# Kernel tuning notes

Hardware: AMD Instinct MI355X
Metric: run time of the kernel (lower is better)

## Reference

```python
import jax, jax.numpy as jnp
import numpy as np


def setup_inputs() -> dict:
    key = jax.random.key(0)
    x = jax.random.normal(key, (16, 64, 256, 256), dtype=jnp.float32)
    return {"x": x}


def reference(x) -> jnp.ndarray:
    B, C, H, W = x.shape
    hw = H * W
    q = x.reshape(B, C, hw)          # proj_query: [B, C, HW]
    k = x.reshape(B, hw, C)          # proj_key: view (reshape), NOT transpose — faithful to source
    attn = jax.nn.softmax(jnp.einsum('bcn,bnd->bcd', q, k), axis=-1)  # [B, C, C]
    out = jnp.einsum('bcd,bdn->bcn', attn, q).reshape(B, C, H, W)
    return out + x
```

## Files before the change

kernel.cpp:

```cpp
#include <hip/hip_runtime.h>

#define B_   16
#define C_   64
#define HW_  65536
#define CHW_ (C_ * HW_)
#define XSTRIDE 260

typedef short bf16x8 __attribute__((ext_vector_type(8)));
typedef float f32x4v __attribute__((ext_vector_type(4)));

__device__ __forceinline__ unsigned short bfrne(float f) {
    unsigned int u = __float_as_uint(f);
    u += 0x7FFFu + ((u >> 16) & 1u);
    return (unsigned short)(u >> 16);
}
__device__ __forceinline__ float bfdec(unsigned short h) {
    return __uint_as_float((unsigned int)h << 16);
}

__global__ __launch_bounds__(256, 2) void k1_gram(const float* __restrict__ x,
                                                  float* __restrict__ partial,
                                                  int nch, int nb) {
    const int ch  = blockIdx.x;
    const int b   = blockIdx.y;
    const int t   = threadIdx.x;
    const int w   = t >> 6;
    const int l   = t & 63;
    const int g   = l >> 4;
    const int col = l & 15;

    __shared__ float Bs[4][2][2048];

    const float* xb = x + (size_t)b * CHW_;
    const int nq  = nb >> 2;
    const int nw0 = ch * nb + w * nq;
    const int nit = nq >> 5;

#define K1_STAGE(dst, ns)                                                  \
    {                                                                      \
        const float* bsrc = xb + (size_t)(ns) * C_;                        \
        _Pragma("unroll")                                                  \
        for (int i = 0; i < 8; i++) {                                      \
            const int sw = (i >> 1) << 2;                                  \
            const float* gp = bsrc + 256 * i + 64 * (l >> 4)               \
                              + 4 * ((l & 15) ^ sw);                       \
            __builtin_amdgcn_global_load_lds(                              \
                (const __attribute__((address_space(1))) void*)gp,         \
                (__attribute__((address_space(3))) void*)((dst) + 256 * i),\
                16, 0, 0);                                                 \
        }                                                                  \
    }

#define K1_LOADA(AV, ns)                                                   \
    _Pragma("unroll")                                                      \
    for (int ct = 0; ct < 4; ct++) {                                       \
        const float* ap = xb + (size_t)(16 * ct + col) * HW_ + (ns) + 8 * g; \
        *(float4*)&AV[ct][0] = *(const float4*)ap;                         \
        *(float4*)&AV[ct][4] = *(const float4*)(ap + 4);                   \
    }

#define K1_CONVA(AV)                                                       \
    _Pragma("unroll")                                                      \
    for (int ct = 0; ct < 4; ct++)                                         \
        _Pragma("unroll")                                                  \
        for (int j = 0; j < 8; j++) {                                      \
            const unsigned short h = bfrne(AV[ct][j]);                     \
            ahi[ct][j] = (short)h;                                         \
            alo[ct][j] = (short)bfrne(AV[ct][j] - bfdec(h));               \
        }

#define K1_BPHASE(cur)                                                     \
    _Pragma("unroll")                                                      \
    for (int dt = 0; dt < 4; dt++) {                                       \
        const int eo = 16 * (dt ^ g) + col;                                \
        float bv[8];                                                       \
        _Pragma("unroll")                                                  \
        for (int j = 0; j < 8; j++) bv[j] = (cur)[(8 * g + j) * 64 + eo];  \
        bf16x8 bhi, blo;                                                   \
        _Pragma("unroll")                                                  \
        for (int j = 0; j < 8; j++) {                                      \
            const unsigned short h = bfrne(bv[j]);                         \
            bhi[j] = (short)h;                                             \
            blo[j] = (short)bfrne(bv[j] - bfdec(h));                       \
        }                                                                  \
        _Pragma("unroll")                                                  \
        for (int ct = 0; ct < 4; ct++) {                                   \
            acc[ct][dt] = __builtin_amdgcn_mfma_f32_16x16x32_bf16(         \
                ahi[ct], bhi, acc[ct][dt], 0, 0, 0);                       \
            acc[ct][dt] = __builtin_amdgcn_mfma_f32_16x16x32_bf16(         \
                ahi[ct], blo, acc[ct][dt], 0, 0, 0);                       \
            acc[ct][dt] = __builtin_amdgcn_mfma_f32_16x16x32_bf16(         \
                alo[ct], bhi, acc[ct][dt], 0, 0, 0);                       \
        }                                                                  \
    }

    f32x4v acc[4][4];
    #pragma unroll
    for (int ct = 0; ct < 4; ct++)
        #pragma unroll
        for (int dt = 0; dt < 4; dt++) acc[ct][dt] = (f32x4v)(0.f);

    float avA[4][8], avB[4][8];
    bf16x8 ahi[4], alo[4];

    K1_STAGE(Bs[w][0], nw0);
    K1_LOADA(avA, nw0);

    for (int it2 = 0; it2 < nit; it2 += 2) {
        {
            const int ns = nw0 + (it2 << 5);
            K1_LOADA(avB, ns + 32);
            K1_STAGE(Bs[w][1], ns + 32);
            K1_CONVA(avA);
            asm volatile("s_waitcnt vmcnt(16)" ::: "memory");
            K1_BPHASE(Bs[w][0]);
        }
        {
            const int ns = nw0 + ((it2 + 1) << 5);
            if (it2 + 2 < nit) {
                K1_LOADA(avA, ns + 32);
                K1_STAGE(Bs[w][0], ns + 32);
            }
            K1_CONVA(avB);
            if (it2 + 2 < nit) asm volatile("s_waitcnt vmcnt(16)" ::: "memory");
            else               asm volatile("s_waitcnt vmcnt(0)"  ::: "memory");
            K1_BPHASE(Bs[w][1]);
        }
    }
#undef K1_STAGE
#undef K1_LOADA
#undef K1_CONVA
#undef K1_BPHASE

    float* sred = (float*)Bs;
    for (int wr = 0; wr < 4; wr++) {
        if (w == wr) {
            #pragma unroll
            for (int ct = 0; ct < 4; ct++)
                #pragma unroll
                for (int dt = 0; dt < 4; dt++)
                    #pragma unroll
                    for (int r = 0; r < 4; r++) {
                        const int idx = (16 * ct + 4 * g + r) * 64 + 16 * dt + col;
                        if (wr == 0) sred[idx] = acc[ct][dt][r];
                        else         sred[idx] += acc[ct][dt][r];
                    }
        }
        __syncthreads();
    }

    float* pb = partial + (size_t)(b * nch + ch) * 4096;
    for (int i = 4 * t; i < 4096; i += 1024)
        *(float4*)&pb[i] = *(const float4*)&sred[i];
}

__global__ __launch_bounds__(256) void k2_softmax(const float* __restrict__ partial,
                                                  unsigned short* __restrict__ mbf,
                                                  int nch) {
    const int c = blockIdx.x;
    const int b = blockIdx.y;
    const int t = threadIdx.x;
    const int w = t >> 6;
    const int d = t & 63;

    float s = 0.f;
    for (int ch = w; ch < nch; ch += 4)
        s += partial[(size_t)(b * nch + ch) * 4096 + c * 64 + d];

    __shared__ float red[256];
    red[t] = s;
    __syncthreads();
    if (w == 0) {
        s = red[d] + red[64 + d] + red[128 + d] + red[192 + d];
        float m = s;
        #pragma unroll
        for (int off = 32; off > 0; off >>= 1) m = fmaxf(m, __shfl_xor(m, off));
        const float e = expf(s - m);
        float sum = e;
        #pragma unroll
        for (int off = 32; off > 0; off >>= 1) sum += __shfl_xor(sum, off);
        mbf[(size_t)b * 4096 + c * 64 + d] = bfrne(e / sum + (c == d ? 1.f : 0.f));
    }
}

__global__ __launch_bounds__(256, 2) void k3_out(const float* __restrict__ x,
                                                 const unsigned short* __restrict__ mbf,
                                                 float* __restrict__ out) {
    const int nbk = blockIdx.x;
    const int b   = blockIdx.y;
    const int t   = threadIdx.x;
    const int w   = t >> 6;
    const int l   = t & 63;
    const int g   = l >> 4;
    const int col = l & 15;

    __shared__ float Xs[64 * XSTRIDE];

    const int nblk = nbk * 256;
    const float* xb = x + (size_t)b * CHW_;

    #pragma unroll
    for (int i = 0; i < 16; i++) {
        const int d = 16 * w + i;
        const int p = ((d >> 3) & 1) << 2;
        const float* gp = xb + (size_t)d * HW_ + nblk + 4 * (l ^ p);
        __builtin_amdgcn_global_load_lds(
            (const __attribute__((address_space(1))) void*)gp,
            (__attribute__((address_space(3))) void*)(&Xs[d * XSTRIDE]),
            16, 0, 0);
    }

    bf16x8 afr[4][2];
    const unsigned short* mb = mbf + (size_t)b * 4096;
    #pragma unroll
    for (int ct = 0; ct < 4; ct++)
        #pragma unroll
        for (int ks = 0; ks < 2; ks++)
            afr[ct][ks] = *(const bf16x8*)(mb + (16 * ct + col) * 64 + 32 * ks + 8 * g);

    __syncthreads();

    f32x4v acc[4][4];
    #pragma unroll
    for (int ct = 0; ct < 4; ct++)
        #pragma unroll
        for (int nt = 0; nt < 4; nt++)
            acc[ct][nt] = (f32x4v)(0.f);

    const int psw = (g & 1) << 2;

    #pragma unroll
    for (int nt = 0; nt < 4; nt++) {
        const int n  = 64 * w + 16 * nt + col;
        const int cn = n >> 2;
        const int eo = ((cn ^ psw) << 2) + (col & 3);

        bf16x8 bfr[2];
        #pragma unroll
        for (int ks = 0; ks < 2; ks++)
            #pragma unroll
            for (int j = 0; j < 8; j++) {
                const int r = 32 * ks + 8 * g + j;
                bfr[ks][j] = (short)bfrne(Xs[r * XSTRIDE + eo]);
            }

        #pragma unroll
        for (int ct = 0; ct < 4; ct++)
            #pragma unroll
            for (int ks = 0; ks < 2; ks++)
                acc[ct][nt] = __builtin_amdgcn_mfma_f32_16x16x32_bf16(
                    afr[ct][ks], bfr[ks], acc[ct][nt], 0, 0, 0);
    }

    __syncthreads();
    #pragma unroll
    for (int ct = 0; ct < 4; ct++)
        #pragma unroll
        for (int nt = 0; nt < 4; nt++)
            #pragma unroll
            for (int r = 0; r < 4; r++)
                Xs[(16 * ct + 4 * g + r) * XSTRIDE + 64 * w + 16 * nt + col] =
                    acc[ct][nt][r];
    __syncthreads();

    float* ob = out + (size_t)b * CHW_ + nblk;
    #pragma unroll
    for (int i = 0; i < 16; i++) {
        const int row = 16 * w + i;
        const float4 v = *(const float4*)&Xs[row * XSTRIDE + 4 * l];
        *(float4*)(ob + (size_t)row * HW_ + 4 * l) = v;
    }
}

extern "C" void kernel_launch(void* const* d_in, const int* in_sizes, int n_in,
                              void* d_out, int out_size, void* d_ws, size_t ws_size,
                              hipStream_t stream) {
    const float* x = (const float*)d_in[0];
    float* out = (float*)d_out;

    float* wsf          = (float*)d_ws;
    unsigned short* mbf = (unsigned short*)wsf;
    float* partial      = wsf + (size_t)B_ * 4096;

    int nch = 64;
    while (nch > 1) {
        size_t need = (size_t)B_ * 4096 * sizeof(float)
                    + (size_t)B_ * nch * 4096 * sizeof(float);
        if (need <= ws_size) break;
        nch >>= 1;
    }
    const int nb = HW_ / nch;

    k1_gram<<<dim3(nch, B_), 256, 0, stream>>>(x, partial, nch, nb);
    k2_softmax<<<dim3(C_, B_), 256, 0, stream>>>(partial, mbf, nch);
    k3_out<<<dim3(HW_ / 256, B_), 256, 0, stream>>>(x, mbf, out);
}
```

Measured before the change: 195.9 us.

## Halve k3 shared tile to raise occupancy, staging K dimension in two passes

The output kernel's LDS tile is cut from 64 to 32 rows of X. The 64-channel reduction is now loaded and consumed in two 32-row stages, and the epilogue writes the result through LDS in two halves. Launch bounds go from 2 to 3 blocks per CU to use the smaller LDS footprint. The cost is extra barriers, and the second stage's global load is serialized after the first compute pass.

```diff
diff --git a/kernel.cpp b/kernel.cpp
--- a/kernel.cpp
+++ b/kernel.cpp
@@ -183,7 +183,7 @@
     }
 }
 
-__global__ __launch_bounds__(256, 2) void k3_out(const float* __restrict__ x,
+__global__ __launch_bounds__(256, 3) void k3_out(const float* __restrict__ x,
                                                  const unsigned short* __restrict__ mbf,
                                                  float* __restrict__ out) {
     const int nbk = blockIdx.x;
@@ -194,21 +194,25 @@
     const int g   = l >> 4;
     const int col = l & 15;
 
-    __shared__ float Xs[64 * XSTRIDE];
+    __shared__ float Xs[32 * XSTRIDE];
 
     const int nblk = nbk * 256;
     const float* xb = x + (size_t)b * CHW_;
 
-    #pragma unroll
-    for (int i = 0; i < 16; i++) {
-        const int d = 16 * w + i;
-        const int p = ((d >> 3) & 1) << 2;
-        const float* gp = xb + (size_t)d * HW_ + nblk + 4 * (l ^ p);
-        __builtin_amdgcn_global_load_lds(
-            (const __attribute__((address_space(1))) void*)gp,
-            (__attribute__((address_space(3))) void*)(&Xs[d * XSTRIDE]),
-            16, 0, 0);
-    }
+#define K3_STAGE(ks)                                                       \
+    _Pragma("unroll")                                                      \
+    for (int i = 0; i < 8; i++) {                                          \
+        const int dl = 8 * w + i;                                          \
+        const int p  = (w & 1) << 2;                                       \
+        const float* gp = xb + (size_t)(32 * (ks) + dl) * HW_              \
+                          + nblk + 4 * (l ^ p);                            \
+        __builtin_amdgcn_global_load_lds(                                  \
+            (const __attribute__((address_space(1))) void*)gp,             \
+            (__attribute__((address_space(3))) void*)(&Xs[dl * XSTRIDE]),  \
+            16, 0, 0);                                                     \
+    }
+
+    K3_STAGE(0);
 
     bf16x8 afr[4][2];
     const unsigned short* mb = mbf + (size_t)b * 4096;
@@ -218,8 +222,6 @@
         for (int ks = 0; ks < 2; ks++)
             afr[ct][ks] = *(const bf16x8*)(mb + (16 * ct + col) * 64 + 32 * ks + 8 * g);
 
-    __syncthreads();
-
     f32x4v acc[4][4];
     #pragma unroll
     for (int ct = 0; ct < 4; ct++)
@@ -230,45 +232,53 @@
     const int psw = (g & 1) << 2;
 
     #pragma unroll
-    for (int nt = 0; nt < 4; nt++) {
-        const int n  = 64 * w + 16 * nt + col;
-        const int cn = n >> 2;
-        const int eo = ((cn ^ psw) << 2) + (col & 3);
-
-        bf16x8 bfr[2];
-        #pragma unroll
-        for (int ks = 0; ks < 2; ks++)
+    for (int ks = 0; ks < 2; ks++) {
+        if (ks == 1) {
+            __syncthreads();
+            K3_STAGE(1);
+        }
+        __syncthreads();
+
+        #pragma unroll
+        for (int nt = 0; nt < 4; nt++) {
+            const int n  = 64 * w + 16 * nt + col;
+            const int cn = n >> 2;
+            const int eo = ((cn ^ psw) << 2) + (col & 3);
+
+            bf16x8 bfr;
             #pragma unroll
-            for (int j = 0; j < 8; j++) {
-                const int r = 32 * ks + 8 * g + j;
-                bfr[ks][j] = (short)bfrne(Xs[r * XSTRIDE + eo]);
-            }
-
-        #pragma unroll
-        for (int ct = 0; ct < 4; ct++)
+            for (int j = 0; j < 8; j++)
+                bfr[j] = (short)bfrne(Xs[(8 * g + j) * XSTRIDE + eo]);
+
             #pragma unroll
-            for (int ks = 0; ks < 2; ks++)
+            for (int ct = 0; ct < 4; ct++)
                 acc[ct][nt] = __builtin_amdgcn_mfma_f32_16x16x32_bf16(
-                    afr[ct][ks], bfr[ks], acc[ct][nt], 0, 0, 0);
-    }
-
-    __syncthreads();
-    #pragma unroll
-    for (int ct = 0; ct < 4; ct++)
-        #pragma unroll
-        for (int nt = 0; nt < 4; nt++)
+                    afr[ct][ks], bfr, acc[ct][nt], 0, 0, 0);
+        }
+    }
+#undef K3_STAGE
+
+    float* ob = out + (size_t)b * CHW_ + nblk;
+    #pragma unroll
+    for (int half = 0; half < 2; half++) {
+        __syncthreads();
+        #pragma unroll
+        for (int c2 = 0; c2 < 2; c2++) {
+            const int ct = 2 * half + c2;
             #pragma unroll
-            for (int r = 0; r < 4; r++)
-                Xs[(16 * ct + 4 * g + r) * XSTRIDE + 64 * w + 16 * nt + col] =
-                    acc[ct][nt][r];
-    __syncthreads();
-
-    float* ob = out + (size_t)b * CHW_ + nblk;
-    #pragma unroll
-    for (int i = 0; i < 16; i++) {
-        const int row = 16 * w + i;
-        const float4 v = *(const float4*)&Xs[row * XSTRIDE + 4 * l];
-        *(float4*)(ob + (size_t)row * HW_ + 4 * l) = v;
+            for (int nt = 0; nt < 4; nt++)
+                #pragma unroll
+                for (int r = 0; r < 4; r++)
+                    Xs[(16 * c2 + 4 * g + r) * XSTRIDE + 64 * w + 16 * nt + col] =
+                        acc[ct][nt][r];
+        }
+        __syncthreads();
+        #pragma unroll
+        for (int i = 0; i < 8; i++) {
+            const int row = 8 * w + i;
+            const float4 v = *(const float4*)&Xs[row * XSTRIDE + 4 * l];
+            *(float4*)(ob + (size_t)(32 * half + row) * HW_ + 4 * l) = v;
+        }
     }
 }
 
```

Result: no change. 193.8 us (-1.1%).
